# Performance work log

Measured on AMD Instinct MI355X. Metric: run time of the kernel, lower is better.

## Reference

```python
import jax, jax.numpy as jnp
import numpy as np

B, N, NTYPES, MN = 8, 1024, 2, 128
M = NTYPES * MN
BETA, M1, M2 = 8, 16, 4
NFEAT = M1 * M2
H = 128
NGHOST = 64
RMAX, RMIN = 6.0, 0.5
ENER_SHIFT = np.array([[-93.0], [-13.6]], dtype=np.float32)


def setup_inputs() -> dict:
    key = jax.random.key(0)
    ks = jax.random.split(key, 12)
    # displacement vectors with |r| in (1, Rmax-0.2)
    d = jax.random.normal(ks[0], (B, N, M, 3), jnp.float32)
    d = d / jnp.linalg.norm(d, axis=-1, keepdims=True)
    r = jax.random.uniform(ks[1], (B, N, M, 1), jnp.float32, 1.0, RMAX - 0.2)
    rvec = d * r
    list_neigh = jax.random.randint(ks[2], (B, N, NTYPES, MN), 1, N + NGHOST + 1).astype(jnp.int32)
    # sorted type map so per-type concat order matches original atom order
    Imagetype_map = jnp.concatenate([jnp.zeros(N // 2, jnp.int32), jnp.ones(N - N // 2, jnp.int32)])
    c_param = 0.1 * jax.random.normal(ks[3], (NTYPES, NTYPES, M1, BETA), jnp.float32)
    def w(k, shape):
        fan_in = shape[-2]
        return (1.0 / np.sqrt(fan_in)) * jax.random.normal(k, shape, jnp.float32)
    return {
        'list_neigh': list_neigh,
        'Imagetype_map': Imagetype_map,
        'rvec': rvec,
        'c_param': c_param,
        'W0': w(ks[4], (NTYPES, NFEAT, H)), 'b0': jnp.zeros((NTYPES, H), jnp.float32),
        'W1': w(ks[5], (NTYPES, H, H)),     'b1': jnp.zeros((NTYPES, H), jnp.float32),
        'W2': w(ks[6], (NTYPES, H, H)),     'b2': jnp.zeros((NTYPES, H), jnp.float32),
        'Wout': w(ks[7], (NTYPES, H, 1)),   'bout': jnp.asarray(ENER_SHIFT),
    }


def _cheb(u):
    # Chebyshev polynomials T_0..T_{BETA-1}, stacked on last axis
    Ts = [jnp.ones_like(u), u]
    for _ in range(2, BETA):
        Ts.append(2.0 * u * Ts[-1] - Ts[-2])
    return jnp.stack(Ts[:BETA], axis=-1)


def _features(rvec, Imagetype_map, c_param):
    r = jnp.linalg.norm(rvec, axis=-1)                      # (B,N,M)
    valid = r > 1e-6
    r_safe = jnp.where(valid, r, 1.0)
    span = RMAX - RMIN
    u = jnp.clip(2.0 * (r_safe - RMIN) / span - 1.0, -1.0, 1.0)
    fc = jnp.where(valid & (r_safe < RMAX),
                   0.5 * (jnp.cos(jnp.pi * (jnp.clip(r_safe, RMIN, RMAX) - RMIN) / span) + 1.0),
                   0.0)
    T = _cheb(u)                                            # (B,N,M,BETA)
    # per-pair Chebyshev coefficients c[type_i, type_j, m1, k]; neighbor type is the block index
    c_i = c_param[Imagetype_map]                            # (N, NTYPES, M1, BETA)
    c_pair = jnp.repeat(c_i, MN, axis=1)                    # (N, M, M1, BETA)
    g = jnp.einsum('bnmk,nmpk->bnmp', T, c_pair) * fc[..., None]   # (B,N,M,M1)
    unit = rvec / r_safe[..., None]
    q = jnp.concatenate([jnp.ones_like(r_safe)[..., None], unit], axis=-1)  # (B,N,M,4)
    q = q * valid[..., None]
    S = jnp.einsum('bnmp,bnma->bnpa', g, q) / M             # (B,N,M1,4)
    feat = jnp.einsum('bnpa,bnqa->bnpq', S, S[:, :, :M2])   # (B,N,M1,M2)
    return feat.reshape(feat.shape[0], feat.shape[1], NFEAT)


def _normalize(feat, Imagetype_map):
    # per-type StandardScaler over all feat values of atoms of that type (detached)
    means, stds = [], []
    for t in range(NTYPES):
        w = (Imagetype_map == t).astype(feat.dtype)         # (N,)
        cnt = w.sum() * feat.shape[0] * NFEAT
        mu = (feat * w[None, :, None]).sum() / cnt
        var = (((feat - mu) ** 2) * w[None, :, None]).sum() / (cnt - 1.0)
        means.append(mu)
        stds.append(jnp.sqrt(var))
    means = jax.lax.stop_gradient(jnp.stack(means))
    stds = jax.lax.stop_gradient(jnp.stack(stds))
    mt = means[Imagetype_map][None, :, None]
    st = stds[Imagetype_map][None, :, None]
    return (feat - mt) / st


def _fit(feat_n, Imagetype_map, W0, b0, W1, b1, W2, b2, Wout, bout):
    Ei = jnp.zeros(feat_n.shape[:2] + (1,), feat_n.dtype)
    for t in range(NTYPES):
        h = jnp.tanh(feat_n @ W0[t] + b0[t])
        h = jnp.tanh(h @ W1[t] + b1[t]) + h                 # resnet skip (equal dims)
        h = jnp.tanh(h @ W2[t] + b2[t]) + h
        e = h @ Wout[t] + bout[t]                           # (B,N,1)
        Ei = Ei + e * (Imagetype_map == t)[None, :, None]
    return Ei


def reference(list_neigh, Imagetype_map, rvec, c_param, W0, b0, W1, b1, W2, b2, Wout, bout):
    def ei_fn(rv):
        feat = _features(rv, Imagetype_map, c_param)
        feat_n = _normalize(feat, Imagetype_map)
        return _fit(feat_n, Imagetype_map, W0, b0, W1, b1, W2, b2, Wout, bout)

    Ei = ei_fn(rvec)                                        # (B,N,1)
    Etot = Ei.sum(axis=1)                                   # (B,1)

    # forces / virial: dE/d rij, scatter-add to center & neighbor atoms (incl. ghosts)
    dEdr = jax.grad(lambda rv: ei_fn(rv).sum())(rvec)       # (B,N,M,3)
    Force = jnp.zeros((B, N + NGHOST, 3), rvec.dtype)
    Force = Force.at[:, :N].add(dEdr.sum(axis=2))           # center atoms: F_i = +sum_j dE/drij
    nl = list_neigh.reshape(B, N, M)
    valid = nl > 0
    j = jnp.where(valid, nl - 1, 0)
    flat_idx = (jnp.arange(B)[:, None, None] * (N + NGHOST) + j).reshape(-1)
    contrib = jnp.where(valid[..., None], -dEdr, 0.0).reshape(-1, 3)
    Force = Force.reshape(-1, 3).at[flat_idx].add(contrib).reshape(B, N + NGHOST, 3)
    Virial = -jnp.einsum('bnma,bnmc->bac', rvec, dEdr).reshape(B, 9)
    return (Etot, Ei.squeeze(-1), Force, Virial)
```

## Files before the change

kernel.cpp:

```cpp
#include <hip/hip_runtime.h>
#include <math.h>

#define BB 8
#define NN 1024
#define MM 256
#define BETA 8
#define M1 16
#define NFEAT 64
#define HH 128
#define NTOT 1088
#define F3 (NTOT*3)
#define RMINf 0.5f
#define SPANf 5.5f
#define PIf 3.14159265358979323846f

#define OUT_EI 8
#define OUT_FORCE 8200
#define OUT_VIR 34312

#define NG2 128
#define AT2 (NN/NG2)

#define MT 16
#define AS0 68
#define AS1 132

#define WS_S     0
#define WS_DF    (WS_S + 8192*64)
#define WS_FP    (WS_DF + 8192*64)
#define WS_STATP (WS_FP + BB*NG2*F3)
#define WS_VIRP  (WS_STATP + 8192*2)
#define WS_WTB   (WS_VIRP + BB*NG2*9)
#define WS_WB    (WS_WTB + 40960)
#define WT0_OFF  0
#define WT1_OFF  16384
#define WT2_OFF  49152

typedef __attribute__((ext_vector_type(8))) short bf8;
typedef __attribute__((ext_vector_type(4))) float f4;

__device__ __forceinline__ float ftanh(float x) {
  const float e = __expf(2.0f*x);
  return 1.0f - 2.0f/(e + 1.0f);
}
__device__ __forceinline__ short f2bs(float f) {
  unsigned u = __float_as_uint(f);
  return (short)((u + 0x7FFFu + ((u >> 16) & 1u)) >> 16);
}
__device__ __forceinline__ bf8 a_frag(const float* p) {
  bf8 a;
  #pragma unroll
  for (int i = 0; i < 8; ++i) a[i] = f2bs(p[i]);
  return a;
}
__device__ __forceinline__ f4 splat4(float v) {
  f4 r; r[0] = v; r[1] = v; r[2] = v; r[3] = v; return r;
}
__device__ __forceinline__ float dpp_wave_sum(float x) {
  x += __int_as_float(__builtin_amdgcn_update_dpp(0, __float_as_int(x), 0x111, 0xf, 0xf, true));
  x += __int_as_float(__builtin_amdgcn_update_dpp(0, __float_as_int(x), 0x112, 0xf, 0xf, true));
  x += __int_as_float(__builtin_amdgcn_update_dpp(0, __float_as_int(x), 0x114, 0xf, 0xf, true));
  x += __int_as_float(__builtin_amdgcn_update_dpp(0, __float_as_int(x), 0x118, 0xf, 0xf, true));
  x += __int_as_float(__builtin_amdgcn_update_dpp(0, __float_as_int(x), 0x142, 0xf, 0xf, true));
  x += __int_as_float(__builtin_amdgcn_update_dpp(0, __float_as_int(x), 0x143, 0xf, 0xf, true));
  return x;
}

__global__ __launch_bounds__(256) void k_feat(
    const float* __restrict__ rvec, const int* __restrict__ tmap,
    const float* __restrict__ c_param, float* __restrict__ S_ws,
    float* __restrict__ statp,
    const float* __restrict__ W0, const float* __restrict__ W1,
    const float* __restrict__ W2,
    unsigned short* __restrict__ wtb, unsigned short* __restrict__ wb)
{
  __shared__ float rv[768];
  __shared__ float c_lds[256];
  __shared__ float prod[256*33];
  __shared__ float part[8*32];
  __shared__ float U[2*32];
  __shared__ float S_lds[64];
  const int tid = threadIdx.x;
  if (blockIdx.x >= BB*NN) {
    const int idx = (blockIdx.x - BB*NN)*256 + tid;
    if (idx < 81920) {
      unsigned short v;
      if (idx < 16384) {
        const int t = idx >> 13, rem = idx & 8191;
        const int j = rem >> 6, f = rem & 63;
        v = (unsigned short)f2bs(W0[t*8192 + f*128 + j]);
      } else if (idx < 49152) {
        const int i = idx - 16384;
        const int t = i >> 14, rem = i & 16383;
        const int j = rem >> 7, f = rem & 127;
        v = (unsigned short)f2bs(W1[t*16384 + f*128 + j]);
      } else {
        const int i = idx - 49152;
        const int t = i >> 14, rem = i & 16383;
        const int j = rem >> 7, f = rem & 127;
        v = (unsigned short)f2bs(W2[t*16384 + f*128 + j]);
      }
      wtb[idx] = v;
    } else {
      const int k = idx - 81920;
      float src;
      if (k < 16384) src = W0[k];
      else if (k < 49152) src = W1[k - 16384];
      else src = W2[k - 49152];
      wb[k] = (unsigned short)f2bs(src);
    }
    return;
  }
  const int bn = blockIdx.x;
  const int n = bn & (NN-1);
  const int ti = tmap[n];
  c_lds[tid] = c_param[ti*256 + tid];
  const float* rb = rvec + (size_t)bn*MM*3;
  rv[tid] = rb[tid]; rv[tid+256] = rb[tid+256]; rv[tid+512] = rb[tid+512];
  __syncthreads();
  const int m = tid;
  const float x = rv[3*m], y = rv[3*m+1], z = rv[3*m+2];
  const float r = sqrtf(x*x + y*y + z*z);
  const float inv_r = 1.0f / r;
  const float ux = x*inv_r, uy = y*inv_r, uz = z*inv_r;
  float u = 2.0f*(r - RMINf)/SPANf - 1.0f;
  u = fminf(fmaxf(u, -1.0f), 1.0f);
  const float fc = 0.5f*(__cosf(PIf*(r - RMINf)/SPANf) + 1.0f);
  float T[BETA];
  T[0] = 1.0f; T[1] = u;
  #pragma unroll
  for (int k = 2; k < BETA; ++k) T[k] = 2.0f*u*T[k-1] - T[k-2];
  float* pr = &prod[m*33];
  #pragma unroll
  for (int k = 0; k < BETA; ++k) {
    const float ft = fc*T[k];
    pr[k*4+0] = ft;
    pr[k*4+1] = ft*ux;
    pr[k*4+2] = ft*uy;
    pr[k*4+3] = ft*uz;
  }
  __syncthreads();
  {
    const int c = tid & 31, oct = tid >> 5;
    const int m0 = oct*32;
    float s = 0.f;
    #pragma unroll 8
    for (int i = 0; i < 32; ++i) s += prod[(m0+i)*33 + c];
    part[oct*32 + c] = s;
  }
  __syncthreads();
  if (tid < 64) {
    const int tj = tid >> 5, c = tid & 31;
    U[tid] = part[(tj*4+0)*32+c] + part[(tj*4+1)*32+c]
           + part[(tj*4+2)*32+c] + part[(tj*4+3)*32+c];
  }
  __syncthreads();
  if (tid < 64) {
    const int p = tid >> 2, a = tid & 3;
    float s = 0.f;
    #pragma unroll
    for (int tj = 0; tj < 2; ++tj)
      #pragma unroll
      for (int k = 0; k < 8; ++k)
        s += c_lds[tj*128 + p*8 + k] * U[tj*32 + k*4 + a];
    s *= (1.0f/(float)MM);
    S_lds[tid] = s;
    S_ws[(size_t)bn*64 + tid] = s;
  }
  __syncthreads();
  if (tid < 64) {
    const int p = tid >> 2, q = tid & 3;
    float f = 0.f;
    #pragma unroll
    for (int a = 0; a < 4; ++a) f += S_lds[p*4+a]*S_lds[q*4+a];
    float fs = f, fss = f*f;
    for (int o = 32; o > 0; o >>= 1) { fs += __shfl_down(fs, o); fss += __shfl_down(fss, o); }
    if (tid == 0) { statp[bn*2+0] = fs; statp[bn*2+1] = fss; }
  }
}

__global__ __launch_bounds__(256) void k_mlp(
    const float* __restrict__ S_ws, const int* __restrict__ tmap,
    const float* __restrict__ statp,
    const unsigned short* __restrict__ wtb, const unsigned short* __restrict__ wb,
    const float* __restrict__ b0, const float* __restrict__ b1,
    const float* __restrict__ b2, const float* __restrict__ Wout,
    const float* __restrict__ bout,
    float* __restrict__ dfeat_ws, float* __restrict__ out)
{
  __shared__ float sl[MT*64];
  __shared__ float xb[MT*AS0];
  __shared__ float t0b[MT*AS1];
  __shared__ float h1b[MT*AS1];
  __shared__ float dzb[MT*AS1];
  __shared__ float es[MT];
  __shared__ float srd[8];
  __shared__ float muSd[2];
  const int tb = blockIdx.x;
  const int bn0 = tb*MT;
  const int tid = threadIdx.x;
  const int wave = tid >> 6, lane = tid & 63;
  const int quad = lane >> 4, nI = lane & 15;
  const int t = tmap[bn0 & (NN-1)];
  {
    const float4* src = (const float4*)(S_ws + (size_t)bn0*64);
    ((float4*)sl)[tid] = src[tid];
  }
  {
    float fs = 0.f, fss = 0.f;
    #pragma unroll 4
    for (int i = 0; i < 16; ++i) {
      const int e = i*256 + tid;
      const int b = e >> 9;
      const int n = t*512 + (e & 511);
      const float2 v = *(const float2*)&statp[((size_t)(b*NN + n))*2];
      fs += v.x; fss += v.y;
    }
    for (int o = 32; o > 0; o >>= 1) { fs += __shfl_down(fs, o); fss += __shfl_down(fss, o); }
    if ((tid & 63) == 0) { srd[(tid>>6)*2] = fs; srd[(tid>>6)*2+1] = fss; }
  }
  __syncthreads();
  if (tid == 0) {
    const float S1 = srd[0]+srd[2]+srd[4]+srd[6];
    const float S2 = srd[1]+srd[3]+srd[5]+srd[7];
    const float cnt = 512.0f * (float)BB * (float)NFEAT;
    const float mu = S1/cnt;
    const float var = (S2 - cnt*mu*mu)/(cnt - 1.0f);
    muSd[0] = mu; muSd[1] = sqrtf(fmaxf(var, 1e-20f));
  }
  __syncthreads();
  const float mu = muSd[0];
  const float inv_sd = 1.0f/muSd[1];
  #pragma unroll
  for (int i = 0; i < 4; ++i) {
    const int e = i*256 + tid;
    const int at = e >> 6, f = e & 63;
    const int p = f >> 2, q = f & 3;
    const float* Sr = &sl[at*64];
    float s = 0.f;
    #pragma unroll
    for (int a = 0; a < 4; ++a) s += Sr[p*4+a]*Sr[q*4+a];
    xb[at*AS0 + f] = (s - mu)*inv_sd;
  }
  __syncthreads();

  const int c0 = (wave*2+0)*16 + nI;
  const int c1 = (wave*2+1)*16 + nI;
  f4 acc0, acc1;

  acc0 = splat4(b0[t*HH + c0]);
  acc1 = splat4(b0[t*HH + c1]);
  {
    const unsigned short* B = wtb + WT0_OFF + t*8192;
    #pragma unroll
    for (int s = 0; s < 2; ++s) {
      const bf8 a  = a_frag(&xb[nI*AS0 + s*32 + quad*8]);
      const bf8 bA = *(const bf8*)&B[(size_t)c0*64 + s*32 + quad*8];
      const bf8 bB = *(const bf8*)&B[(size_t)c1*64 + s*32 + quad*8];
      acc0 = __builtin_amdgcn_mfma_f32_16x16x32_bf16(a, bA, acc0, 0, 0, 0);
      acc1 = __builtin_amdgcn_mfma_f32_16x16x32_bf16(a, bB, acc1, 0, 0, 0);
    }
  }
  #pragma unroll
  for (int r = 0; r < 4; ++r) {
    const int row = quad*4 + r;
    t0b[row*AS1 + c0] = ftanh(acc0[r]);
    t0b[row*AS1 + c1] = ftanh(acc1[r]);
  }
  __syncthreads();
  acc0 = splat4(b1[t*HH + c0]);
  acc1 = splat4(b1[t*HH + c1]);
  {
    const unsigned short* B = wtb + WT1_OFF + t*16384;
    #pragma unroll
    for (int s = 0; s < 4; ++s) {
      const bf8 a  = a_frag(&t0b[nI*AS1 + s*32 + quad*8]);
      const bf8 bA = *(const bf8*)&B[(size_t)c0*128 + s*32 + quad*8];
      const bf8 bB = *(const bf8*)&B[(size_t)c1*128 + s*32 + quad*8];
      acc0 = __builtin_amdgcn_mfma_f32_16x16x32_bf16(a, bA, acc0, 0, 0, 0);
      acc1 = __builtin_amdgcn_mfma_f32_16x16x32_bf16(a, bB, acc1, 0, 0, 0);
    }
  }
  #pragma unroll
  for (int r = 0; r < 4; ++r) {
    const int row = quad*4 + r;
    h1b[row*AS1 + c0] = ftanh(acc0[r]) + t0b[row*AS1 + c0];
    h1b[row*AS1 + c1] = ftanh(acc1[r]) + t0b[row*AS1 + c1];
  }
  __syncthreads();
  acc0 = splat4(b2[t*HH + c0]);
  acc1 = splat4(b2[t*HH + c1]);
  {
    const unsigned short* B = wtb + WT2_OFF + t*16384;
    #pragma unroll
    for (int s = 0; s < 4; ++s) {
      const bf8 a  = a_frag(&h1b[nI*AS1 + s*32 + quad*8]);
      const bf8 bA = *(const bf8*)&B[(size_t)c0*128 + s*32 + quad*8];
      const bf8 bB = *(const bf8*)&B[(size_t)c1*128 + s*32 + quad*8];
      acc0 = __builtin_amdgcn_mfma_f32_16x16x32_bf16(a, bA, acc0, 0, 0, 0);
      acc1 = __builtin_amdgcn_mfma_f32_16x16x32_bf16(a, bB, acc1, 0, 0, 0);
    }
  }
  #pragma unroll
  for (int r = 0; r < 4; ++r) {
    const int row = quad*4 + r;
    dzb[row*AS1 + c0] = acc0[r];
    dzb[row*AS1 + c1] = acc1[r];
  }
  __syncthreads();
  {
    const int at = tid >> 4, cb = (tid & 15)*8;
    const float* wop = Wout + t*HH;
    float ep = 0.f;
    #pragma unroll
    for (int j = 0; j < 8; ++j) {
      const int c = cb + j;
      const float z2 = dzb[at*AS1 + c];
      const float t2 = ftanh(z2);
      const float wo = wop[c];
      ep += (t2 + h1b[at*AS1 + c])*wo;
      dzb[at*AS1 + c] = wo*(1.0f - t2*t2);
    }
    ep += __shfl_down(ep, 8, 16);
    ep += __shfl_down(ep, 4, 16);
    ep += __shfl_down(ep, 2, 16);
    ep += __shfl_down(ep, 1, 16);
    if ((tid & 15) == 0) es[at] = ep;
  }
  __syncthreads();
  if (tid < MT) out[OUT_EI + bn0 + tid] = es[tid] + bout[t];

  {
    const float* wop = Wout + t*HH;
    acc0 = splat4(wop[c0]);
    acc1 = splat4(wop[c1]);
    const unsigned short* B = wb + WT2_OFF + t*16384;
    #pragma unroll
    for (int s = 0; s < 4; ++s) {
      const bf8 a  = a_frag(&dzb[nI*AS1 + s*32 + quad*8]);
      const bf8 bA = *(const bf8*)&B[(size_t)c0*128 + s*32 + quad*8];
      const bf8 bB = *(const bf8*)&B[(size_t)c1*128 + s*32 + quad*8];
      acc0 = __builtin_amdgcn_mfma_f32_16x16x32_bf16(a, bA, acc0, 0, 0, 0);
      acc1 = __builtin_amdgcn_mfma_f32_16x16x32_bf16(a, bB, acc1, 0, 0, 0);
    }
  }
  __syncthreads();
  float dh10[4], dh11[4];
  #pragma unroll
  for (int r = 0; r < 4; ++r) {
    const int row = quad*4 + r;
    dh10[r] = acc0[r]; dh11[r] = acc1[r];
    const float t1a = h1b[row*AS1 + c0] - t0b[row*AS1 + c0];
    const float t1b = h1b[row*AS1 + c1] - t0b[row*AS1 + c1];
    dzb[row*AS1 + c0] = acc0[r]*(1.0f - t1a*t1a);
    dzb[row*AS1 + c1] = acc1[r]*(1.0f - t1b*t1b);
  }
  __syncthreads();
  acc0[0]=dh10[0]; acc0[1]=dh10[1]; acc0[2]=dh10[2]; acc0[3]=dh10[3];
  acc1[0]=dh11[0]; acc1[1]=dh11[1]; acc1[2]=dh11[2]; acc1[3]=dh11[3];
  {
    const unsigned short* B = wb + WT1_OFF + t*16384;
    #pragma unroll
    for (int s = 0; s < 4; ++s) {
      const bf8 a  = a_frag(&dzb[nI*AS1 + s*32 + quad*8]);
      const bf8 bA = *(const bf8*)&B[(size_t)c0*128 + s*32 + quad*8];
      const bf8 bB = *(const bf8*)&B[(size_t)c1*128 + s*32 + quad*8];
      acc0 = __builtin_amdgcn_mfma_f32_16x16x32_bf16(a, bA, acc0, 0, 0, 0);
      acc1 = __builtin_amdgcn_mfma_f32_16x16x32_bf16(a, bB, acc1, 0, 0, 0);
    }
  }
  __syncthreads();
  #pragma unroll
  for (int r = 0; r < 4; ++r) {
    const int row = quad*4 + r;
    const float ta = t0b[row*AS1 + c0], tb = t0b[row*AS1 + c1];
    dzb[row*AS1 + c0] = acc0[r]*(1.0f - ta*ta);
    dzb[row*AS1 + c1] = acc1[r]*(1.0f - tb*tb);
  }
  __syncthreads();
  {
    const int cx = wave*16 + nI;
    acc0 = splat4(0.f);
    const unsigned short* B = wb + WT0_OFF + t*8192;
    #pragma unroll
    for (int s = 0; s < 4; ++s) {
      const bf8 a  = a_frag(&dzb[nI*AS1 + s*32 + quad*8]);
      const bf8 bA = *(const bf8*)&B[(size_t)cx*128 + s*32 + quad*8];
      acc0 = __builtin_amdgcn_mfma_f32_16x16x32_bf16(a, bA, acc0, 0, 0, 0);
    }
    #pragma unroll
    for (int r = 0; r < 4; ++r)
      dfeat_ws[(size_t)(bn0 + quad*4 + r)*64 + cx] = acc0[r]*inv_sd;
  }
}

__global__ __launch_bounds__(256, 4) void k_bwdsc(
    const float* __restrict__ rvec, const int* __restrict__ nlist,
    const int* __restrict__ tmap, const float* __restrict__ c_param,
    const float* __restrict__ S_ws, const float* __restrict__ dfeat_ws,
    float* __restrict__ fpart_ws, float* __restrict__ virp)
{
  __shared__ float c_lds[256];
  __shared__ float Sb[AT2*64];
  __shared__ float Db[AT2*64];
  __shared__ float dSb[AT2*64];
  __shared__ float Eb[AT2*64];
  __shared__ float fpart[F3];
  __shared__ float wredc[AT2*4*3];
  __shared__ float vred[4*9];
  const int blk = blockIdx.x;
  const int b = blk >> 7;
  const int g = blk & (NG2-1);
  const int n0 = g*AT2;
  const int tid = threadIdx.x;
  const int ti = tmap[n0];
  c_lds[tid] = c_param[ti*256 + tid];
  if (tid < 128) {
    const float4* s4 = (const float4*)(S_ws + ((size_t)b*NN + n0)*64);
    const float4* d4 = (const float4*)(dfeat_ws + ((size_t)b*NN + n0)*64);
    ((float4*)Sb)[tid] = s4[tid];
    ((float4*)Db)[tid] = d4[tid];
  }
  {
    const float4 z4 = {0.f, 0.f, 0.f, 0.f};
    for (int i = tid; i < F3/4; i += 256) ((float4*)fpart)[i] = z4;
  }
  __syncthreads();
  #pragma unroll
  for (int it = 0; it < 2; ++it) {
    const int idx = it*256 + tid;
    const int at = idx >> 6, f = idx & 63;
    const int i = f >> 2, a = f & 3;
    const float* Sr = &Sb[at*64];
    const float* Dr = &Db[at*64];
    float v = 0.f;
    #pragma unroll
    for (int q = 0; q < 4; ++q) v += Dr[i*4+q]*Sr[q*4+a];
    if (i < 4)
      for (int p = 0; p < 16; ++p) v += Dr[p*4+i]*Sr[p*4+a];
    dSb[idx] = v;
  }
  __syncthreads();
  #pragma unroll
  for (int it = 0; it < 2; ++it) {
    const int idx = it*256 + tid;
    const int at = idx >> 6, rem = idx & 63;
    const int tj = rem >> 5, a = (rem >> 3) & 3, k = rem & 7;
    float e = 0.f;
    #pragma unroll
    for (int p = 0; p < 16; ++p) e += dSb[at*64 + p*4 + a]*c_lds[tj*128 + p*8 + k];
    Eb[idx] = e;
  }
  __syncthreads();

  float vir[9];
  #pragma unroll
  for (int i = 0; i < 9; ++i) vir[i] = 0.f;
  const int wave = tid >> 6, lane = tid & 63;
  const int tjm = tid >> 7;
  const float dudr = 2.0f/SPANf;
  const float invM = 1.0f/(float)MM;

  const size_t rowbase = ((size_t)b*NN + n0)*MM;
  float px0, py0, pz0, px1, py1, pz1; int pnl0, pnl1;
  {
    const float* rp0 = rvec + (rowbase + tid)*3;
    const float* rp1 = rvec + (rowbase + MM + tid)*3;
    px0 = rp0[0]; py0 = rp0[1]; pz0 = rp0[2]; pnl0 = nlist[rowbase + tid];
    px1 = rp1[0]; py1 = rp1[1]; pz1 = rp1[2]; pnl1 = nlist[rowbase + MM + tid];
  }
  for (int a0 = 0; a0 < AT2; a0 += 2) {
    const float x0 = px0, y0 = py0, z0 = pz0; const int nl0 = pnl0;
    const float x1 = px1, y1 = py1, z1 = pz1; const int nl1 = pnl1;
    if (a0 + 2 < AT2) {
      const float* rp0 = rvec + (rowbase + (size_t)(a0+2)*MM + tid)*3;
      const float* rp1 = rvec + (rowbase + (size_t)(a0+3)*MM + tid)*3;
      px0 = rp0[0]; py0 = rp0[1]; pz0 = rp0[2];
      pnl0 = nlist[rowbase + (size_t)(a0+2)*MM + tid];
      px1 = rp1[0]; py1 = rp1[1]; pz1 = rp1[2];
      pnl1 = nlist[rowbase + (size_t)(a0+3)*MM + tid];
    }
    float Er0[32], Er1[32];
    {
      const float4* p0 = (const float4*)&Eb[a0*64 + tjm*32];
      const float4* p1 = (const float4*)&Eb[(a0+1)*64 + tjm*32];
      #pragma unroll
      for (int q = 0; q < 8; ++q) {
        const float4 v0 = p0[q], v1 = p1[q];
        Er0[q*4+0]=v0.x; Er0[q*4+1]=v0.y; Er0[q*4+2]=v0.z; Er0[q*4+3]=v0.w;
        Er1[q*4+0]=v1.x; Er1[q*4+1]=v1.y; Er1[q*4+2]=v1.z; Er1[q*4+3]=v1.w;
      }
    }
    const float r_0 = sqrtf(x0*x0 + y0*y0 + z0*z0);
    const float r_1 = sqrtf(x1*x1 + y1*y1 + z1*z1);
    const float ir0 = 1.0f/r_0, ir1 = 1.0f/r_1;
    const float ux0 = x0*ir0, uy0 = y0*ir0, uz0 = z0*ir0;
    const float ux1 = x1*ir1, uy1 = y1*ir1, uz1 = z1*ir1;
    float u0 = 2.0f*(r_0 - RMINf)/SPANf - 1.0f;
    float u1 = 2.0f*(r_1 - RMINf)/SPANf - 1.0f;
    u0 = fminf(fmaxf(u0, -1.0f), 1.0f);
    u1 = fminf(fmaxf(u1, -1.0f), 1.0f);
    float s0a, c0a, s1a, c1a;
    __sincosf(PIf*(r_0 - RMINf)/SPANf, &s0a, &c0a);
    __sincosf(PIf*(r_1 - RMINf)/SPANf, &s1a, &c1a);
    const float fc0 = 0.5f*(c0a + 1.0f), dfc0 = -0.5f*(PIf/SPANf)*s0a;
    const float fc1 = 0.5f*(c1a + 1.0f), dfc1 = -0.5f*(PIf/SPANf)*s1a;
    float ta0[4], tda0[4], ta1[4], tda1[4];
    #pragma unroll
    for (int aa = 0; aa < 4; ++aa) {
      ta0[aa]  = Er0[aa*8] + Er0[aa*8+1]*u0;
      tda0[aa] = Er0[aa*8+1];
      ta1[aa]  = Er1[aa*8] + Er1[aa*8+1]*u1;
      tda1[aa] = Er1[aa*8+1];
    }
    float t0m2 = 1.f, t0m1 = u0, d0m2 = 0.f, d0m1 = 1.f;
    float t1m2 = 1.f, t1m1 = u1, d1m2 = 0.f, d1m1 = 1.f;
    #pragma unroll
    for (int k = 2; k < BETA; ++k) {
      const float tk0 = 2.f*u0*t0m1 - t0m2;
      const float dk0 = 2.f*t0m1 + 2.f*u0*d0m1 - d0m2;
      const float tk1 = 2.f*u1*t1m1 - t1m2;
      const float dk1 = 2.f*t1m1 + 2.f*u1*d1m1 - d1m2;
      #pragma unroll
      for (int aa = 0; aa < 4; ++aa) {
        ta0[aa]  += Er0[aa*8+k]*tk0;
        tda0[aa] += Er0[aa*8+k]*dk0;
        ta1[aa]  += Er1[aa*8+k]*tk1;
        tda1[aa] += Er1[aa*8+k]*dk1;
      }
      t0m2 = t0m1; t0m1 = tk0; d0m2 = d0m1; d0m1 = dk0;
      t1m2 = t1m1; t1m1 = tk1; d1m2 = d1m1; d1m1 = dk1;
    }
    float A0 = dfc0*(ta0[0] + ux0*ta0[1] + uy0*ta0[2] + uz0*ta0[3])
             + fc0*dudr*(tda0[0] + ux0*tda0[1] + uy0*tda0[2] + uz0*tda0[3]);
    float A1 = dfc1*(ta1[0] + ux1*ta1[1] + uy1*ta1[2] + uz1*ta1[3])
             + fc1*dudr*(tda1[0] + ux1*tda1[1] + uy1*tda1[2] + uz1*tda1[3]);
    float q10 = fc0*ta0[1], q20 = fc0*ta0[2], q30 = fc0*ta0[3];
    float q11 = fc1*ta1[1], q21 = fc1*ta1[2], q31 = fc1*ta1[3];
    A0 *= invM; q10 *= invM; q20 *= invM; q30 *= invM;
    A1 *= invM; q11 *= invM; q21 *= invM; q31 *= invM;
    const float qu0 = q10*ux0 + q20*uy0 + q30*uz0;
    const float qu1 = q11*ux1 + q21*uy1 + q31*uz1;
    const float d00 = A0*ux0 + (q10 - qu0*ux0)*ir0;
    const float d01 = A0*uy0 + (q20 - qu0*uy0)*ir0;
    const float d02 = A0*uz0 + (q30 - qu0*uz0)*ir0;
    const float d10 = A1*ux1 + (q11 - qu1*ux1)*ir1;
    const float d11 = A1*uy1 + (q21 - qu1*uy1)*ir1;
    const float d12 = A1*uz1 + (q31 - qu1*uz1)*ir1;
    if (nl0 > 0) {
      const int j = nl0 - 1;
      atomicAdd(&fpart[j*3+0], -d00);
      atomicAdd(&fpart[j*3+1], -d01);
      atomicAdd(&fpart[j*3+2], -d02);
    }
    if (nl1 > 0) {
      const int j = nl1 - 1;
      atomicAdd(&fpart[j*3+0], -d10);
      atomicAdd(&fpart[j*3+1], -d11);
      atomicAdd(&fpart[j*3+2], -d12);
    }
    vir[0] -= x0*d00 + x1*d10; vir[1] -= x0*d01 + x1*d11; vir[2] -= x0*d02 + x1*d12;
    vir[3] -= y0*d00 + y1*d10; vir[4] -= y0*d01 + y1*d11; vir[5] -= y0*d02 + y1*d12;
    vir[6] -= z0*d00 + z1*d10; vir[7] -= z0*d01 + z1*d11; vir[8] -= z0*d02 + z1*d12;
    const float r00 = dpp_wave_sum(d00), r01 = dpp_wave_sum(d01), r02 = dpp_wave_sum(d02);
    const float r10 = dpp_wave_sum(d10), r11 = dpp_wave_sum(d11), r12 = dpp_wave_sum(d12);
    if (lane == 63) {
      wredc[(a0*4 + wave)*3 + 0] = r00;
      wredc[(a0*4 + wave)*3 + 1] = r01;
      wredc[(a0*4 + wave)*3 + 2] = r02;
      wredc[((a0+1)*4 + wave)*3 + 0] = r10;
      wredc[((a0+1)*4 + wave)*3 + 1] = r11;
      wredc[((a0+1)*4 + wave)*3 + 2] = r12;
    }
  }
  #pragma unroll
  for (int i = 0; i < 9; ++i) {
    const float v = dpp_wave_sum(vir[i]);
    if (lane == 63) vred[wave*9 + i] = v;
  }
  __syncthreads();
  if (tid < AT2*3) {
    const int at = tid/3, c = tid - at*3;
    const float v = wredc[(at*4+0)*3+c] + wredc[(at*4+1)*3+c]
                  + wredc[(at*4+2)*3+c] + wredc[(at*4+3)*3+c];
    atomicAdd(&fpart[(n0+at)*3 + c], v);
  }
  if (tid >= 64 && tid < 73) {
    const int i = tid - 64;
    virp[(size_t)blk*9 + i] = vred[i] + vred[9+i] + vred[18+i] + vred[27+i];
  }
  __syncthreads();
  {
    float* dst = fpart_ws + (size_t)blk*F3;
    for (int i = tid; i < F3/4; i += 256)
      ((float4*)dst)[i] = ((float4*)fpart)[i];
  }
}

__global__ __launch_bounds__(256) void k_reduce(
    const float* __restrict__ fpart_ws, const float* __restrict__ virp,
    float* __restrict__ out)
{
  __shared__ float comb[4*64];
  __shared__ float red[4];
  const int tid = threadIdx.x;
  const int blk = blockIdx.x;
  if (blk < 408) {
    const int el = tid & 63, gc = tid >> 6;
    const int e = blk*64 + el;
    const int b = e / F3;
    const int i = e - b*F3;
    const float* base = fpart_ws + (size_t)(b*NG2)*F3 + i;
    float s = 0.f;
    #pragma unroll 8
    for (int g = gc*32; g < gc*32 + 32; ++g) s += base[(size_t)g*F3];
    comb[gc*64 + el] = s;
    __syncthreads();
    if (tid < 64)
      out[OUT_FORCE + blk*64 + tid] = comb[tid] + comb[64+tid] + comb[128+tid] + comb[192+tid];
    return;
  }
  if (blk < 480) {
    const int vb = blk - 408;
    const int b = vb / 9, c = vb - (vb/9)*9;
    float v = (tid < NG2) ? virp[((size_t)(b*NG2 + tid))*9 + c] : 0.f;
    for (int o = 32; o > 0; o >>= 1) v += __shfl_down(v, o);
    if ((tid & 63) == 0) red[tid >> 6] = v;
    __syncthreads();
    if (tid == 0) out[OUT_VIR + vb] = red[0] + red[1];
    return;
  }
  const int b = blk - 480;
  float v = 0.f;
  #pragma unroll
  for (int k = 0; k < 4; ++k) v += out[OUT_EI + b*NN + k*256 + tid];
  for (int o = 32; o > 0; o >>= 1) v += __shfl_down(v, o);
  if ((tid & 63) == 0) red[tid >> 6] = v;
  __syncthreads();
  if (tid == 0) out[b] = red[0] + red[1] + red[2] + red[3];
}

extern "C" void kernel_launch(void* const* d_in, const int* in_sizes, int n_in,
                              void* d_out, int out_size, void* d_ws, size_t ws_size,
                              hipStream_t stream)
{
  const int*   nlist = (const int*)d_in[0];
  const int*   tmap  = (const int*)d_in[1];
  const float* rvec  = (const float*)d_in[2];
  const float* cpar  = (const float*)d_in[3];
  const float* W0 = (const float*)d_in[4];
  const float* b0 = (const float*)d_in[5];
  const float* W1 = (const float*)d_in[6];
  const float* b1 = (const float*)d_in[7];
  const float* W2 = (const float*)d_in[8];
  const float* b2 = (const float*)d_in[9];
  const float* Wout = (const float*)d_in[10];
  const float* bout = (const float*)d_in[11];
  float* out = (float*)d_out;
  float* ws = (float*)d_ws;
  float* S_ws   = ws + WS_S;
  float* df_ws  = ws + WS_DF;
  float* fpartw = ws + WS_FP;
  float* statp  = ws + WS_STATP;
  float* virp   = ws + WS_VIRP;
  unsigned short* wtb = (unsigned short*)(ws + WS_WTB);
  unsigned short* wb  = (unsigned short*)(ws + WS_WB);

  k_feat <<<BB*NN + 640, 256, 0, stream>>>(rvec, tmap, cpar, S_ws, statp,
                                           W0, W1, W2, wtb, wb);
  k_mlp  <<<(BB*NN)/MT, 256, 0, stream>>>(S_ws, tmap, statp, wtb, wb,
                                          b0, b1, b2, Wout, bout, df_ws, out);
  k_bwdsc<<<BB*NG2, 256, 0, stream>>>(rvec, nlist, tmap, cpar, S_ws, df_ws,
                                      fpartw, virp);
  k_reduce<<<488, 256, 0, stream>>>(fpartw, virp, out);
}
```

Measured before the change: 171.5 us.

## Double k_bwdsc block size to 512 threads, splitting atoms across halves

The backward scatter kernel now runs 512 threads per block. Each half of the block processes 4 of the 8 atoms in the group, and the setup loops drop from two iterations to one. The goal is more parallelism per block, shorter per-thread serial loops, and more waves to hide memory latency. In exchange, the launch bound asks for 8 blocks of 512 threads, which may force register spilling given the large per-thread arrays.

```diff
diff --git a/kernel.cpp b/kernel.cpp
--- a/kernel.cpp
+++ b/kernel.cpp
@@ -394,7 +394,7 @@
   }
 }
 
-__global__ __launch_bounds__(256, 4) void k_bwdsc(
+__global__ __launch_bounds__(512, 8) void k_bwdsc(
     const float* __restrict__ rvec, const int* __restrict__ nlist,
     const int* __restrict__ tmap, const float* __restrict__ c_param,
     const float* __restrict__ S_ws, const float* __restrict__ dfeat_ws,
@@ -407,14 +407,16 @@
   __shared__ float Eb[AT2*64];
   __shared__ float fpart[F3];
   __shared__ float wredc[AT2*4*3];
-  __shared__ float vred[4*9];
+  __shared__ float vred[8*9];
   const int blk = blockIdx.x;
   const int b = blk >> 7;
   const int g = blk & (NG2-1);
   const int n0 = g*AT2;
   const int tid = threadIdx.x;
+  const int m = tid & 255;
+  const int h = tid >> 8;
   const int ti = tmap[n0];
-  c_lds[tid] = c_param[ti*256 + tid];
+  if (tid < 256) c_lds[tid] = c_param[ti*256 + tid];
   if (tid < 128) {
     const float4* s4 = (const float4*)(S_ws + ((size_t)b*NN + n0)*64);
     const float4* d4 = (const float4*)(dfeat_ws + ((size_t)b*NN + n0)*64);
@@ -423,12 +425,11 @@
   }
   {
     const float4 z4 = {0.f, 0.f, 0.f, 0.f};
-    for (int i = tid; i < F3/4; i += 256) ((float4*)fpart)[i] = z4;
-  }
-  __syncthreads();
-  #pragma unroll
-  for (int it = 0; it < 2; ++it) {
-    const int idx = it*256 + tid;
+    for (int i = tid; i < F3/4; i += 512) ((float4*)fpart)[i] = z4;
+  }
+  __syncthreads();
+  {
+    const int idx = tid;
     const int at = idx >> 6, f = idx & 63;
     const int i = f >> 2, a = f & 3;
     const float* Sr = &Sb[at*64];
@@ -441,9 +442,8 @@
     dSb[idx] = v;
   }
   __syncthreads();
-  #pragma unroll
-  for (int it = 0; it < 2; ++it) {
-    const int idx = it*256 + tid;
+  {
+    const int idx = tid;
     const int at = idx >> 6, rem = idx & 63;
     const int tj = rem >> 5, a = (rem >> 3) & 3, k = rem & 7;
     float e = 0.f;
@@ -457,28 +457,34 @@
   #pragma unroll
   for (int i = 0; i < 9; ++i) vir[i] = 0.f;
   const int wave = tid >> 6, lane = tid & 63;
-  const int tjm = tid >> 7;
+  const int w4 = wave & 3;
+  const int tjm = (tid >> 7) & 1;
   const float dudr = 2.0f/SPANf;
   const float invM = 1.0f/(float)MM;
 
   const size_t rowbase = ((size_t)b*NN + n0)*MM;
+  const int abase = h*4;
   float px0, py0, pz0, px1, py1, pz1; int pnl0, pnl1;
   {
-    const float* rp0 = rvec + (rowbase + tid)*3;
-    const float* rp1 = rvec + (rowbase + MM + tid)*3;
-    px0 = rp0[0]; py0 = rp0[1]; pz0 = rp0[2]; pnl0 = nlist[rowbase + tid];
-    px1 = rp1[0]; py1 = rp1[1]; pz1 = rp1[2]; pnl1 = nlist[rowbase + MM + tid];
-  }
-  for (int a0 = 0; a0 < AT2; a0 += 2) {
+    const float* rp0 = rvec + (rowbase + (size_t)abase*MM + m)*3;
+    const float* rp1 = rvec + (rowbase + (size_t)(abase+1)*MM + m)*3;
+    px0 = rp0[0]; py0 = rp0[1]; pz0 = rp0[2];
+    pnl0 = nlist[rowbase + (size_t)abase*MM + m];
+    px1 = rp1[0]; py1 = rp1[1]; pz1 = rp1[2];
+    pnl1 = nlist[rowbase + (size_t)(abase+1)*MM + m];
+  }
+  #pragma unroll
+  for (int it = 0; it < 2; ++it) {
+    const int a0 = abase + it*2;
     const float x0 = px0, y0 = py0, z0 = pz0; const int nl0 = pnl0;
     const float x1 = px1, y1 = py1, z1 = pz1; const int nl1 = pnl1;
-    if (a0 + 2 < AT2) {
-      const float* rp0 = rvec + (rowbase + (size_t)(a0+2)*MM + tid)*3;
-      const float* rp1 = rvec + (rowbase + (size_t)(a0+3)*MM + tid)*3;
+    if (it == 0) {
+      const float* rp0 = rvec + (rowbase + (size_t)(abase+2)*MM + m)*3;
+      const float* rp1 = rvec + (rowbase + (size_t)(abase+3)*MM + m)*3;
       px0 = rp0[0]; py0 = rp0[1]; pz0 = rp0[2];
-      pnl0 = nlist[rowbase + (size_t)(a0+2)*MM + tid];
+      pnl0 = nlist[rowbase + (size_t)(abase+2)*MM + m];
       px1 = rp1[0]; py1 = rp1[1]; pz1 = rp1[2];
-      pnl1 = nlist[rowbase + (size_t)(a0+3)*MM + tid];
+      pnl1 = nlist[rowbase + (size_t)(abase+3)*MM + m];
     }
     float Er0[32], Er1[32];
     {
@@ -565,12 +571,12 @@
     const float r00 = dpp_wave_sum(d00), r01 = dpp_wave_sum(d01), r02 = dpp_wave_sum(d02);
     const float r10 = dpp_wave_sum(d10), r11 = dpp_wave_sum(d11), r12 = dpp_wave_sum(d12);
     if (lane == 63) {
-      wredc[(a0*4 + wave)*3 + 0] = r00;
-      wredc[(a0*4 + wave)*3 + 1] = r01;
-      wredc[(a0*4 + wave)*3 + 2] = r02;
-      wredc[((a0+1)*4 + wave)*3 + 0] = r10;
-      wredc[((a0+1)*4 + wave)*3 + 1] = r11;
-      wredc[((a0+1)*4 + wave)*3 + 2] = r12;
+      wredc[(a0*4 + w4)*3 + 0] = r00;
+      wredc[(a0*4 + w4)*3 + 1] = r01;
+      wredc[(a0*4 + w4)*3 + 2] = r02;
+      wredc[((a0+1)*4 + w4)*3 + 0] = r10;
+      wredc[((a0+1)*4 + w4)*3 + 1] = r11;
+      wredc[((a0+1)*4 + w4)*3 + 2] = r12;
     }
   }
   #pragma unroll
@@ -587,12 +593,15 @@
   }
   if (tid >= 64 && tid < 73) {
     const int i = tid - 64;
-    virp[(size_t)blk*9 + i] = vred[i] + vred[9+i] + vred[18+i] + vred[27+i];
+    float s = 0.f;
+    #pragma unroll
+    for (int w = 0; w < 8; ++w) s += vred[w*9 + i];
+    virp[(size_t)blk*9 + i] = s;
   }
   __syncthreads();
   {
     float* dst = fpart_ws + (size_t)blk*F3;
-    for (int i = tid; i < F3/4; i += 256)
+    for (int i = tid; i < F3/4; i += 512)
       ((float4*)dst)[i] = ((float4*)fpart)[i];
   }
 }
@@ -670,7 +679,7 @@
                                            W0, W1, W2, wtb, wb);
   k_mlp  <<<(BB*NN)/MT, 256, 0, stream>>>(S_ws, tmap, statp, wtb, wb,
                                           b0, b1, b2, Wout, bout, df_ws, out);
-  k_bwdsc<<<BB*NG2, 256, 0, stream>>>(rvec, nlist, tmap, cpar, S_ws, df_ws,
+  k_bwdsc<<<BB*NG2, 512, 0, stream>>>(rvec, nlist, tmap, cpar, S_ws, df_ws,
                                       fpartw, virp);
   k_reduce<<<488, 256, 0, stream>>>(fpartw, virp, out);
 }
```

After: 182.2 us. 1.06x slower.

## Map one atom per wavefront in feature kernel with DPP register reductions

Applied to the files above, without the earlier changes.

The feature kernel now handles four atoms per block, one per wavefront. Each lane accumulates the 32 Chebyshev-moment terms in registers over its neighbours, and the sums are reduced across the wave with DPP instead of being staged through a large LDS product array behind several block barriers. This removes the LDS traffic and syncthreads overhead and cuts the grid from 8192 to 2048 feature blocks. In exchange, each lane holds 32 accumulators in registers, runs 32 DPP reductions per half, and reads rvec with strided per-lane global loads that are not staged in LDS.

```diff
diff --git a/kernel.cpp b/kernel.cpp
--- a/kernel.cpp
+++ b/kernel.cpp
@@ -25,6 +25,8 @@
 #define AS0 68
 #define AS1 132
 
+#define FEAT_BLKS 2048
+
 #define WS_S     0
 #define WS_DF    (WS_S + 8192*64)
 #define WS_FP    (WS_DF + 8192*64)
@@ -74,15 +76,9 @@
     const float* __restrict__ W2,
     unsigned short* __restrict__ wtb, unsigned short* __restrict__ wb)
 {
-  __shared__ float rv[768];
-  __shared__ float c_lds[256];
-  __shared__ float prod[256*33];
-  __shared__ float part[8*32];
-  __shared__ float U[2*32];
-  __shared__ float S_lds[64];
   const int tid = threadIdx.x;
-  if (blockIdx.x >= BB*NN) {
-    const int idx = (blockIdx.x - BB*NN)*256 + tid;
+  if (blockIdx.x >= FEAT_BLKS) {
+    const int idx = (blockIdx.x - FEAT_BLKS)*256 + tid;
     if (idx < 81920) {
       unsigned short v;
       if (idx < 16384) {
@@ -111,71 +107,82 @@
     }
     return;
   }
-  const int bn = blockIdx.x;
+  __shared__ float cA[512];
+  __shared__ float Ubuf[4*64];
+  __shared__ float Slds[4*64];
+  cA[tid] = c_param[tid];
+  cA[256 + tid] = c_param[256 + tid];
+  __syncthreads();
+
+  const int wave = tid >> 6, lane = tid & 63;
+  const int bn = blockIdx.x*4 + wave;
   const int n = bn & (NN-1);
   const int ti = tmap[n];
-  c_lds[tid] = c_param[ti*256 + tid];
   const float* rb = rvec + (size_t)bn*MM*3;
-  rv[tid] = rb[tid]; rv[tid+256] = rb[tid+256]; rv[tid+512] = rb[tid+512];
-  __syncthreads();
-  const int m = tid;
-  const float x = rv[3*m], y = rv[3*m+1], z = rv[3*m+2];
-  const float r = sqrtf(x*x + y*y + z*z);
-  const float inv_r = 1.0f / r;
-  const float ux = x*inv_r, uy = y*inv_r, uz = z*inv_r;
-  float u = 2.0f*(r - RMINf)/SPANf - 1.0f;
-  u = fminf(fmaxf(u, -1.0f), 1.0f);
-  const float fc = 0.5f*(__cosf(PIf*(r - RMINf)/SPANf) + 1.0f);
-  float T[BETA];
-  T[0] = 1.0f; T[1] = u;
-  #pragma unroll
-  for (int k = 2; k < BETA; ++k) T[k] = 2.0f*u*T[k-1] - T[k-2];
-  float* pr = &prod[m*33];
-  #pragma unroll
-  for (int k = 0; k < BETA; ++k) {
-    const float ft = fc*T[k];
-    pr[k*4+0] = ft;
-    pr[k*4+1] = ft*ux;
-    pr[k*4+2] = ft*uy;
-    pr[k*4+3] = ft*uz;
-  }
-  __syncthreads();
-  {
-    const int c = tid & 31, oct = tid >> 5;
-    const int m0 = oct*32;
-    float s = 0.f;
-    #pragma unroll 8
-    for (int i = 0; i < 32; ++i) s += prod[(m0+i)*33 + c];
-    part[oct*32 + c] = s;
-  }
-  __syncthreads();
-  if (tid < 64) {
-    const int tj = tid >> 5, c = tid & 31;
-    U[tid] = part[(tj*4+0)*32+c] + part[(tj*4+1)*32+c]
-           + part[(tj*4+2)*32+c] + part[(tj*4+3)*32+c];
-  }
-  __syncthreads();
-  if (tid < 64) {
-    const int p = tid >> 2, a = tid & 3;
+
+  #pragma unroll
+  for (int half = 0; half < 2; ++half) {
+    float acc[32];
+    #pragma unroll
+    for (int c = 0; c < 32; ++c) acc[c] = 0.f;
+    #pragma unroll
+    for (int s = 0; s < 2; ++s) {
+      const int m = half*128 + s*64 + lane;
+      const float x = rb[3*m], y = rb[3*m+1], z = rb[3*m+2];
+      const float r = sqrtf(x*x + y*y + z*z);
+      const float ir = 1.0f/r;
+      const float ux = x*ir, uy = y*ir, uz = z*ir;
+      float u = 2.0f*(r - RMINf)/SPANf - 1.0f;
+      u = fminf(fmaxf(u, -1.0f), 1.0f);
+      const float fc = 0.5f*(__cosf(PIf*(r - RMINf)/SPANf) + 1.0f);
+      float tm2 = 1.0f, tm1 = u;
+      acc[0] += fc;  acc[1] += fc*ux;  acc[2] += fc*uy;  acc[3] += fc*uz;
+      {
+        const float ft = fc*u;
+        acc[4] += ft; acc[5] += ft*ux; acc[6] += ft*uy; acc[7] += ft*uz;
+      }
+      #pragma unroll
+      for (int k = 2; k < BETA; ++k) {
+        const float tk = 2.0f*u*tm1 - tm2;
+        const float ft = fc*tk;
+        acc[k*4+0] += ft;
+        acc[k*4+1] += ft*ux;
+        acc[k*4+2] += ft*uy;
+        acc[k*4+3] += ft*uz;
+        tm2 = tm1; tm1 = tk;
+      }
+    }
+    #pragma unroll
+    for (int c = 0; c < 32; ++c) acc[c] = dpp_wave_sum(acc[c]);
+    if (lane == 63) {
+      float* Uw = &Ubuf[wave*64 + half*32];
+      #pragma unroll
+      for (int c = 0; c < 32; ++c) Uw[c] = acc[c];
+    }
+  }
+  {
+    const int p = lane >> 2, a = lane & 3;
+    const float* Uw = &Ubuf[wave*64];
+    const float* cw = &cA[ti*256];
     float s = 0.f;
     #pragma unroll
     for (int tj = 0; tj < 2; ++tj)
       #pragma unroll
       for (int k = 0; k < 8; ++k)
-        s += c_lds[tj*128 + p*8 + k] * U[tj*32 + k*4 + a];
+        s += cw[tj*128 + p*8 + k] * Uw[tj*32 + k*4 + a];
     s *= (1.0f/(float)MM);
-    S_lds[tid] = s;
-    S_ws[(size_t)bn*64 + tid] = s;
-  }
-  __syncthreads();
-  if (tid < 64) {
-    const int p = tid >> 2, q = tid & 3;
+    Slds[wave*64 + lane] = s;
+    S_ws[(size_t)bn*64 + lane] = s;
+  }
+  {
+    const int p = lane >> 2, q = lane & 3;
+    const float* Sw = &Slds[wave*64];
     float f = 0.f;
     #pragma unroll
-    for (int a = 0; a < 4; ++a) f += S_lds[p*4+a]*S_lds[q*4+a];
+    for (int a = 0; a < 4; ++a) f += Sw[p*4+a]*Sw[q*4+a];
     float fs = f, fss = f*f;
     for (int o = 32; o > 0; o >>= 1) { fs += __shfl_down(fs, o); fss += __shfl_down(fss, o); }
-    if (tid == 0) { statp[bn*2+0] = fs; statp[bn*2+1] = fss; }
+    if (lane == 0) { statp[bn*2+0] = fs; statp[bn*2+1] = fss; }
   }
 }
 
@@ -666,8 +673,8 @@
   unsigned short* wtb = (unsigned short*)(ws + WS_WTB);
   unsigned short* wb  = (unsigned short*)(ws + WS_WB);
 
-  k_feat <<<BB*NN + 640, 256, 0, stream>>>(rvec, tmap, cpar, S_ws, statp,
-                                           W0, W1, W2, wtb, wb);
+  k_feat <<<FEAT_BLKS + 640, 256, 0, stream>>>(rvec, tmap, cpar, S_ws, statp,
+                                               W0, W1, W2, wtb, wb);
   k_mlp  <<<(BB*NN)/MT, 256, 0, stream>>>(S_ws, tmap, statp, wtb, wb,
                                           b0, b1, b2, Wout, bout, df_ws, out);
   k_bwdsc<<<BB*NG2, 256, 0, stream>>>(rvec, nlist, tmap, cpar, S_ws, df_ws,
```

Measured after the change: 169.5 us. About the same (-1.2%).
